# Kernel optimization log

Measured on AMD Instinct MI355X. Metric: run time of the kernel, lower is better.

Reference implementation:

```python
import jax, jax.numpy as jnp
import numpy as np

DIM = 512
HID = 4 * DIM
E = 8
B, T = 2, 2048


def setup_inputs() -> dict:
    key = jax.random.key(0)
    ks = jax.random.split(key, 8)
    s = 0.02
    x = jax.random.normal(ks[0], (B, T, DIM), dtype=jnp.float32)
    route = jax.random.randint(ks[1], (B * T,), 0, E, dtype=jnp.int32)
    # stacked per-expert params; Linear y = x @ W + b with W in [in, out] layout
    w_in = jax.random.normal(ks[2], (E, DIM, HID), dtype=jnp.float32) * s
    b_in = jnp.zeros((E, HID), dtype=jnp.float32)
    w_gate = jax.random.normal(ks[3], (E, DIM, HID), dtype=jnp.float32) * s
    b_gate = jnp.zeros((E, HID), dtype=jnp.float32)
    w_out = jax.random.normal(ks[4], (E, HID, DIM), dtype=jnp.float32) * s
    b_out = jnp.zeros((E, DIM), dtype=jnp.float32)
    return {"x": x, "route": route, "w_in": w_in, "b_in": b_in,
            "w_gate": w_gate, "b_gate": b_gate, "w_out": w_out, "b_out": b_out}


def reference(x, route, w_in, b_in, w_gate, b_gate, w_out, b_out):
    Bb, Tt, C = x.shape
    xf = x.reshape(-1, C)  # [N, C]
    out = jnp.zeros_like(xf)
    n_experts = w_in.shape[0]
    # loop over the small fixed expert set; each expert is a SwiGLU FFN,
    # output scattered back by masking (same math as output[idx] += expert(x[idx]))
    for e in range(n_experts):
        mask = (route == e).astype(xf.dtype)[:, None]  # [N, 1]
        h = jax.nn.silu(xf @ w_gate[e] + b_gate[e]) * (xf @ w_in[e] + b_in[e])  # [N, 4C]
        out = out + mask * (h @ w_out[e] + b_out[e])
    return out.reshape(Bb, Tt, C)
```

## Files before the change

### kernel.cpp

```cpp
#include <hip/hip_runtime.h>

#define DIM 512
#define HID 2048
#define NEXP 8

typedef __attribute__((ext_vector_type(8))) short v8s;
typedef __attribute__((ext_vector_type(4))) float v4f;

__device__ __forceinline__ unsigned short f2bf(float f) {
  union { __bf16 b; unsigned short u; } c;
  c.b = (__bf16)f;
  return c.u;
}

__device__ __forceinline__ void gload16(const void* g, void* l) {
  __builtin_amdgcn_global_load_lds(
      (const __attribute__((address_space(1))) unsigned int*)g,
      (__attribute__((address_space(3))) unsigned int*)l, 16, 0, 0);
}

__global__ void route_prep(const int* __restrict__ route, int* __restrict__ meta, int ntok) {
  __shared__ int c[NEXP];
  int t = threadIdx.x;
  if (t < NEXP) c[t] = 0;
  __syncthreads();
  for (int n = t; n < ntok; n += blockDim.x) atomicAdd(&c[route[n]], 1);
  __syncthreads();
  if (t == 0) {
    int acc = 0, pacc = 0;
    for (int e = 0; e < NEXP; ++e) {
      meta[e] = c[e];
      meta[NEXP + e] = acc;
      meta[2 * NEXP + e] = acc;
      meta[3 * NEXP + e] = pacc;
      acc += c[e];
      pacc += ((c[e] + 127) >> 7) << 7;
    }
  }
}

__global__ void fill_perm(const int* __restrict__ route, int* __restrict__ meta,
                          int* __restrict__ perm, int ntok) {
  int n = blockIdx.x * blockDim.x + threadIdx.x;
  if (n < ntok) {
    int p = atomicAdd(&meta[2 * NEXP + route[n]], 1);
    perm[p] = n;
  }
}


__global__ __launch_bounds__(256) void wgi_conv(
    const float* __restrict__ wg, const float* __restrict__ wi,
    unsigned short* __restrict__ wgp, unsigned short* __restrict__ wip)
{
  const int s = blockIdx.x;
  const int j = blockIdx.y;
  const int e = blockIdx.z >> 1;
  const int which = blockIdx.z & 1;
  const float* src = (which ? wi : wg) + (size_t)e * DIM * HID;
  unsigned short* dst = (which ? wip : wgp) + (((size_t)e * 16 + j) * 8 + s) * 8192;
  const int t = threadIdx.x;
  #pragma unroll
  for (int i = 0; i < 4; ++i) {
    const int c = t + 256 * i;
    const int kq = c >> 7, n = c & 127;
    const float* srow = src + (size_t)(s * 64 + kq * 8) * HID + j * 128 + n;
    v8s r;
    #pragma unroll
    for (int q = 0; q < 8; ++q) r[q] = (short)f2bf(srow[(size_t)q * HID]);
    *(v8s*)(dst + (size_t)c * 8) = r;
  }
}

__global__ __launch_bounds__(256) void wo_conv(
    const float* __restrict__ wo, unsigned short* __restrict__ wop)
{
  const int s = blockIdx.x;
  const int j = blockIdx.y;
  const int e = blockIdx.z;
  const float* src = wo + (size_t)e * HID * DIM;
  unsigned short* dst = wop + (((size_t)e * 8 + j) * 32 + s) * 4096;
  const int t = threadIdx.x;
  #pragma unroll
  for (int i = 0; i < 2; ++i) {
    const int c = t + 256 * i;
    const int kq = c >> 6, n = c & 63;
    const float* srow = src + (size_t)(s * 64 + kq * 8) * DIM + j * 64 + n;
    v8s r;
    #pragma unroll
    for (int q = 0; q < 8; ++q) r[q] = (short)f2bf(srow[(size_t)q * DIM]);
    *(v8s*)(dst + (size_t)c * 8) = r;
  }
}

__global__ __launch_bounds__(256, 2) void gemm1(
    const float* __restrict__ x,
    const unsigned short* __restrict__ wgp, const float* __restrict__ bg_,
    const unsigned short* __restrict__ wip, const float* __restrict__ bi_,
    const int* __restrict__ meta, const int* __restrict__ perm,
    unsigned short* __restrict__ hbuf)
{
  const int bid = blockIdx.x;
  const int e = bid & 7;
  const int r_ = bid >> 3;
  const int j = r_ & 15;
  const int mt = r_ >> 4;
  const int cnt = meta[e];
  const int m0 = mt * 128;
  if (m0 >= cnt) return;
  const int off  = meta[NEXP + e];
  const int poff = meta[3 * NEXP + e];
  const int n0 = j * 128;

  __shared__ __align__(16) unsigned char lds[49152];

  const int t = threadIdx.x;
  const int l = t & 63, w = t >> 6;
  const int wm = w >> 1, wn = w & 1;
  const int fr = l & 15, fg = l >> 4;

  const int ar = t >> 1, ah = t & 1;
  int arow = m0 + ar; if (arow >= cnt) arow = cnt - 1;
  const float* asrc = x + (size_t)perm[off + arow] * DIM + ah * 16;

  const unsigned short* pg = wgp + ((size_t)e * 16 + j) * 65536;
  const unsigned short* pi = wip + ((size_t)e * 16 + j) * 65536;

  v4f accG[4][4], accI[4][4];
  #pragma unroll
  for (int i = 0; i < 4; ++i)
    #pragma unroll
    for (int q = 0; q < 4; ++q) {
      accG[i][q] = (v4f){0.f, 0.f, 0.f, 0.f};
      accI[i][q] = (v4f){0.f, 0.f, 0.f, 0.f};
    }

  auto stage_w = [&](int s, int b) {
    unsigned char* base = lds + b * 24576;
    const unsigned short* pgs = pg + (size_t)s * 4096;
    const unsigned short* pis = pi + (size_t)s * 4096;
    gload16(pgs + t * 8,        base + 8192 + w * 1024);
    gload16(pgs + 2048 + t * 8, base + 8192 + 4096 + w * 1024);
    gload16(pis + t * 8,        base + 16384 + w * 1024);
    gload16(pis + 2048 + t * 8, base + 16384 + 4096 + w * 1024);
  };

  float4 a0, a1, a2, a3;
  auto stage_a_load = [&](int s) {
    const float4* p = (const float4*)(asrc + s * 32);
    a0 = p[0]; a1 = p[1]; a2 = p[2]; a3 = p[3];
  };
  auto stage_a_write = [&](int b) {
    unsigned char* base = lds + b * 24576;
    v8s r0, r1;
    r0[0] = (short)f2bf(a0.x); r0[1] = (short)f2bf(a0.y);
    r0[2] = (short)f2bf(a0.z); r0[3] = (short)f2bf(a0.w);
    r0[4] = (short)f2bf(a1.x); r0[5] = (short)f2bf(a1.y);
    r0[6] = (short)f2bf(a1.z); r0[7] = (short)f2bf(a1.w);
    r1[0] = (short)f2bf(a2.x); r1[1] = (short)f2bf(a2.y);
    r1[2] = (short)f2bf(a2.z); r1[3] = (short)f2bf(a2.w);
    r1[4] = (short)f2bf(a3.x); r1[5] = (short)f2bf(a3.y);
    r1[6] = (short)f2bf(a3.z); r1[7] = (short)f2bf(a3.w);
    *(v8s*)(base + ((ah * 2 + 0) * 128 + ar) * 16) = r0;
    *(v8s*)(base + ((ah * 2 + 1) * 128 + ar) * 16) = r1;
  };

  stage_w(0, 0);
  stage_a_load(0);
  stage_a_write(0);
  __syncthreads();

  int cur = 0;
  for (int s = 0; s < 16; ++s) {
    if (s < 15) {
      stage_w(s + 1, cur ^ 1);
      stage_a_load(s + 1);
    }
    unsigned char* base = lds + cur * 24576;
    v8s af[4], gf[4], inf[4];
    #pragma unroll
    for (int mf = 0; mf < 4; ++mf)
      af[mf] = *(const v8s*)(base + (fg * 128 + wm * 64 + mf * 16 + fr) * 16);
    #pragma unroll
    for (int nf = 0; nf < 4; ++nf) {
      gf[nf]  = *(const v8s*)(base + 8192  + (fg * 128 + wn * 64 + nf * 16 + fr) * 16);
      inf[nf] = *(const v8s*)(base + 16384 + (fg * 128 + wn * 64 + nf * 16 + fr) * 16);
    }
    #pragma unroll
    for (int mf = 0; mf < 4; ++mf)
      #pragma unroll
      for (int nf = 0; nf < 4; ++nf) {
        accG[mf][nf] = __builtin_amdgcn_mfma_f32_16x16x32_bf16(af[mf], gf[nf],  accG[mf][nf], 0, 0, 0);
        accI[mf][nf] = __builtin_amdgcn_mfma_f32_16x16x32_bf16(af[mf], inf[nf], accI[mf][nf], 0, 0, 0);
      }
    if (s < 15) stage_a_write(cur ^ 1);
    __syncthreads();
    cur ^= 1;
  }

  #pragma unroll
  for (int nf = 0; nf < 4; ++nf) {
    const int c = n0 + wn * 64 + nf * 16 + fr;
    const float bg = bg_[(size_t)e * HID + c];
    const float bi = bi_[(size_t)e * HID + c];
    #pragma unroll
    for (int mf = 0; mf < 4; ++mf)
      #pragma unroll
      for (int jj = 0; jj < 4; ++jj) {
        const int r = wm * 64 + mf * 16 + fg * 4 + jj;
        if (m0 + r < cnt) {
          const float g = accG[mf][nf][jj] + bg;
          const float v = accI[mf][nf][jj] + bi;
          const float hval = g / (1.f + __expf(-g)) * v;
          const int grow = poff + m0 + r;
          hbuf[(size_t)(grow >> 6) * 131072 + ((size_t)(c >> 3) * 64 + (grow & 63)) * 8 + (c & 7)] = f2bf(hval);
        }
      }
  }
}

__global__ __launch_bounds__(256, 4) void gemm2(
    const unsigned short* __restrict__ hbuf,
    const unsigned short* __restrict__ wop, const float* __restrict__ bo_,
    const int* __restrict__ meta, const int* __restrict__ perm,
    float* __restrict__ out)
{
  const int bid = blockIdx.x;
  const int e = bid & 7;
  const int r_ = bid >> 3;
  const int jn = r_ & 7;
  const int mt = r_ >> 3;
  const int cnt = meta[e];
  const int m0 = mt * 64;
  if (m0 >= cnt) return;
  const int off  = meta[NEXP + e];
  const int poff = meta[3 * NEXP + e];
  const int n0 = jn * 64;

  __shared__ __align__(16) unsigned char lds[32768];

  const int t = threadIdx.x;
  const int l = t & 63, w = t >> 6;
  const int wm = w >> 1, wn = w & 1;
  const int fr = l & 15, fg = l >> 4;

  const unsigned short* pa = hbuf + (size_t)((poff + m0) >> 6) * 131072;
  const unsigned short* pb = wop + ((size_t)e * 8 + jn) * 131072;

  v4f acc[2][2];
  #pragma unroll
  for (int i = 0; i < 2; ++i)
    #pragma unroll
    for (int q = 0; q < 2; ++q) acc[i][q] = (v4f){0.f, 0.f, 0.f, 0.f};

  auto stage = [&](int s, int b) {
    unsigned char* base = lds + b * 16384;
    const unsigned short* pas = pa + (size_t)s * 4096;
    const unsigned short* pbs = pb + (size_t)s * 4096;
    gload16(pas + t * 8,        base + w * 1024);
    gload16(pas + 2048 + t * 8, base + 4096 + w * 1024);
    gload16(pbs + t * 8,        base + 8192 + w * 1024);
    gload16(pbs + 2048 + t * 8, base + 8192 + 4096 + w * 1024);
  };

  stage(0, 0);
  __syncthreads();

  int cur = 0;
  for (int s = 0; s < 32; ++s) {
    if (s < 31) stage(s + 1, cur ^ 1);
    unsigned char* base = lds + cur * 16384;
    v8s af[2][2], bf2[2][2];
    #pragma unroll
    for (int kk = 0; kk < 2; ++kk) {
      #pragma unroll
      for (int mf = 0; mf < 2; ++mf)
        af[kk][mf]  = *(const v8s*)(base + ((kk * 4 + fg) * 64 + wm * 32 + mf * 16 + fr) * 16);
      #pragma unroll
      for (int nf = 0; nf < 2; ++nf)
        bf2[kk][nf] = *(const v8s*)(base + 8192 + ((kk * 4 + fg) * 64 + wn * 32 + nf * 16 + fr) * 16);
    }
    #pragma unroll
    for (int kk = 0; kk < 2; ++kk)
      #pragma unroll
      for (int mf = 0; mf < 2; ++mf)
        #pragma unroll
        for (int nf = 0; nf < 2; ++nf)
          acc[mf][nf] = __builtin_amdgcn_mfma_f32_16x16x32_bf16(af[kk][mf], bf2[kk][nf], acc[mf][nf], 0, 0, 0);
    __syncthreads();
    cur ^= 1;
  }

  #pragma unroll
  for (int nf = 0; nf < 2; ++nf) {
    const int c = n0 + wn * 32 + nf * 16 + fr;
    const float bo = bo_[(size_t)e * DIM + c];
    #pragma unroll
    for (int mf = 0; mf < 2; ++mf)
      #pragma unroll
      for (int jj = 0; jj < 4; ++jj) {
        const int r = wm * 32 + mf * 16 + fg * 4 + jj;
        if (m0 + r < cnt)
          out[(size_t)perm[off + m0 + r] * DIM + c] = acc[mf][nf][jj] + bo;
      }
  }
}

extern "C" void kernel_launch(void* const* d_in, const int* in_sizes, int n_in,
                              void* d_out, int out_size, void* d_ws, size_t ws_size,
                              hipStream_t stream) {
  const float* x      = (const float*)d_in[0];
  const int*   route  = (const int*)d_in[1];
  const float* w_in   = (const float*)d_in[2];
  const float* b_in   = (const float*)d_in[3];
  const float* w_gate = (const float*)d_in[4];
  const float* b_gate = (const float*)d_in[5];
  const float* w_out  = (const float*)d_in[6];
  const float* b_out  = (const float*)d_in[7];
  float* out = (float*)d_out;

  const int ntok = in_sizes[1];

  int* meta = (int*)d_ws;
  int* perm = (int*)((char*)d_ws + 128);

  const size_t WGP_OFF = 32768;
  const size_t WMAT_BYTES = (size_t)NEXP * DIM * HID * 2;

  unsigned short* wgp  = (unsigned short*)((char*)d_ws + WGP_OFF);
  unsigned short* wip  = (unsigned short*)((char*)d_ws + WGP_OFF + WMAT_BYTES);
  unsigned short* wop  = (unsigned short*)((char*)d_ws + WGP_OFF + 2 * WMAT_BYTES);
  unsigned short* hbuf = (unsigned short*)((char*)d_ws + WGP_OFF + 3 * WMAT_BYTES);

  const int MT1 = (ntok + 127) / 128;
  const int MT2 = (ntok + 63) / 64;

  route_prep<<<1, 256, 0, stream>>>(route, meta, ntok);
  fill_perm<<<(ntok + 255) / 256, 256, 0, stream>>>(route, meta, perm, ntok);
  wgi_conv<<<dim3(8, 16, 16), 256, 0, stream>>>(w_gate, w_in, wgp, wip);
  wo_conv<<<dim3(32, 8, 8), 256, 0, stream>>>(w_out, wop);
  gemm1<<<NEXP * 16 * MT1, 256, 0, stream>>>(
      x, wgp, b_gate, wip, b_in, meta, perm, hbuf);
  gemm2<<<NEXP * 8 * MT2, 256, 0, stream>>>(
      hbuf, wop, b_out, meta, perm, out);
}
```

Before: 126.2 us.

## Pre-gather tokens to bf16, shrink gemm1 M tile, widen gemm2 to 8 waves

Adds an x_conv kernel that gathers the routed tokens and converts them to packed bf16 once, so gemm1 can stream A through async global-to-LDS loads instead of per-block fp32 loads and conversions. gemm1 drops from 128-row to 64-row tiles with a smaller LDS footprint and higher occupancy bound, giving more blocks. gemm2 now runs 512 threads with one n-fragment per wave. The xp buffer reuses the wop workspace, so wo_conv is reordered to run after gemm1, which serialises that conversion behind the first GEMM.

Measured after the change: 112.9 us. -10.5%, faster.

```diff
diff --git a/kernel.cpp b/kernel.cpp
--- a/kernel.cpp
+++ b/kernel.cpp
@@ -93,11 +93,40 @@
   }
 }
 
-__global__ __launch_bounds__(256, 2) void gemm1(
-    const float* __restrict__ x,
+__global__ __launch_bounds__(256) void x_conv(
+    const float* __restrict__ x, const int* __restrict__ meta,
+    const int* __restrict__ perm, unsigned short* __restrict__ xp)
+{
+  const int bid = blockIdx.x;
+  const int e = bid & 7;
+  const int mt = bid >> 3;
+  const int cnt = meta[e];
+  if (mt * 64 >= cnt) return;
+  const int off  = meta[NEXP + e];
+  const int poff = meta[3 * NEXP + e];
+  const int t = threadIdx.x;
+  const int r = t & 63, q = t >> 6;
+  int arow = mt * 64 + r; if (arow >= cnt) arow = cnt - 1;
+  const float* src = x + (size_t)perm[off + arow] * DIM + q * 128;
+  unsigned short* dst = xp + (size_t)((poff + mt * 64) >> 6) * 32768;
+  #pragma unroll
+  for (int j = 0; j < 16; ++j) {
+    float4 f0 = ((const float4*)src)[2 * j];
+    float4 f1 = ((const float4*)src)[2 * j + 1];
+    v8s v;
+    v[0] = (short)f2bf(f0.x); v[1] = (short)f2bf(f0.y);
+    v[2] = (short)f2bf(f0.z); v[3] = (short)f2bf(f0.w);
+    v[4] = (short)f2bf(f1.x); v[5] = (short)f2bf(f1.y);
+    v[6] = (short)f2bf(f1.z); v[7] = (short)f2bf(f1.w);
+    *(v8s*)(dst + (size_t)((q * 16 + j) * 64 + r) * 8) = v;
+  }
+}
+
+__global__ __launch_bounds__(256, 4) void gemm1(
+    const unsigned short* __restrict__ xp,
     const unsigned short* __restrict__ wgp, const float* __restrict__ bg_,
     const unsigned short* __restrict__ wip, const float* __restrict__ bi_,
-    const int* __restrict__ meta, const int* __restrict__ perm,
+    const int* __restrict__ meta,
     unsigned short* __restrict__ hbuf)
 {
   const int bid = blockIdx.x;
@@ -106,120 +135,89 @@
   const int j = r_ & 15;
   const int mt = r_ >> 4;
   const int cnt = meta[e];
-  const int m0 = mt * 128;
+  const int m0 = mt * 64;
   if (m0 >= cnt) return;
-  const int off  = meta[NEXP + e];
   const int poff = meta[3 * NEXP + e];
   const int n0 = j * 128;
 
-  __shared__ __align__(16) unsigned char lds[49152];
+  __shared__ __align__(16) unsigned char lds[40960];
 
   const int t = threadIdx.x;
   const int l = t & 63, w = t >> 6;
   const int wm = w >> 1, wn = w & 1;
   const int fr = l & 15, fg = l >> 4;
 
-  const int ar = t >> 1, ah = t & 1;
-  int arow = m0 + ar; if (arow >= cnt) arow = cnt - 1;
-  const float* asrc = x + (size_t)perm[off + arow] * DIM + ah * 16;
-
+  const unsigned short* pa = xp + (size_t)((poff + m0) >> 6) * 32768;
   const unsigned short* pg = wgp + ((size_t)e * 16 + j) * 65536;
   const unsigned short* pi = wip + ((size_t)e * 16 + j) * 65536;
 
-  v4f accG[4][4], accI[4][4];
-  #pragma unroll
-  for (int i = 0; i < 4; ++i)
+  v4f accG[2][4], accI[2][4];
+  #pragma unroll
+  for (int i = 0; i < 2; ++i)
     #pragma unroll
     for (int q = 0; q < 4; ++q) {
       accG[i][q] = (v4f){0.f, 0.f, 0.f, 0.f};
       accI[i][q] = (v4f){0.f, 0.f, 0.f, 0.f};
     }
 
-  auto stage_w = [&](int s, int b) {
-    unsigned char* base = lds + b * 24576;
-    const unsigned short* pgs = pg + (size_t)s * 4096;
-    const unsigned short* pis = pi + (size_t)s * 4096;
-    gload16(pgs + t * 8,        base + 8192 + w * 1024);
-    gload16(pgs + 2048 + t * 8, base + 8192 + 4096 + w * 1024);
-    gload16(pis + t * 8,        base + 16384 + w * 1024);
-    gload16(pis + 2048 + t * 8, base + 16384 + 4096 + w * 1024);
+  auto stage = [&](int s, int b) {
+    unsigned char* base = lds + b * 20480;
+    gload16(pa + (size_t)s * 2048 + t * 8,        base + w * 1024);
+    gload16(pg + (size_t)s * 4096 + t * 8,        base + 4096 + w * 1024);
+    gload16(pg + (size_t)s * 4096 + 2048 + t * 8, base + 8192 + w * 1024);
+    gload16(pi + (size_t)s * 4096 + t * 8,        base + 12288 + w * 1024);
+    gload16(pi + (size_t)s * 4096 + 2048 + t * 8, base + 16384 + w * 1024);
   };
 
-  float4 a0, a1, a2, a3;
-  auto stage_a_load = [&](int s) {
-    const float4* p = (const float4*)(asrc + s * 32);
-    a0 = p[0]; a1 = p[1]; a2 = p[2]; a3 = p[3];
-  };
-  auto stage_a_write = [&](int b) {
-    unsigned char* base = lds + b * 24576;
-    v8s r0, r1;
-    r0[0] = (short)f2bf(a0.x); r0[1] = (short)f2bf(a0.y);
-    r0[2] = (short)f2bf(a0.z); r0[3] = (short)f2bf(a0.w);
-    r0[4] = (short)f2bf(a1.x); r0[5] = (short)f2bf(a1.y);
-    r0[6] = (short)f2bf(a1.z); r0[7] = (short)f2bf(a1.w);
-    r1[0] = (short)f2bf(a2.x); r1[1] = (short)f2bf(a2.y);
-    r1[2] = (short)f2bf(a2.z); r1[3] = (short)f2bf(a2.w);
-    r1[4] = (short)f2bf(a3.x); r1[5] = (short)f2bf(a3.y);
-    r1[6] = (short)f2bf(a3.z); r1[7] = (short)f2bf(a3.w);
-    *(v8s*)(base + ((ah * 2 + 0) * 128 + ar) * 16) = r0;
-    *(v8s*)(base + ((ah * 2 + 1) * 128 + ar) * 16) = r1;
-  };
-
-  stage_w(0, 0);
-  stage_a_load(0);
-  stage_a_write(0);
+  stage(0, 0);
   __syncthreads();
 
   int cur = 0;
   for (int s = 0; s < 16; ++s) {
-    if (s < 15) {
-      stage_w(s + 1, cur ^ 1);
-      stage_a_load(s + 1);
-    }
-    unsigned char* base = lds + cur * 24576;
-    v8s af[4], gf[4], inf[4];
-    #pragma unroll
-    for (int mf = 0; mf < 4; ++mf)
-      af[mf] = *(const v8s*)(base + (fg * 128 + wm * 64 + mf * 16 + fr) * 16);
+    if (s < 15) stage(s + 1, cur ^ 1);
+    unsigned char* base = lds + cur * 20480;
+    v8s af[2], gf[4], inf[4];
+    #pragma unroll
+    for (int mf = 0; mf < 2; ++mf)
+      af[mf] = *(const v8s*)(base + ((fg * 64) + wm * 32 + mf * 16 + fr) * 16);
     #pragma unroll
     for (int nf = 0; nf < 4; ++nf) {
-      gf[nf]  = *(const v8s*)(base + 8192  + (fg * 128 + wn * 64 + nf * 16 + fr) * 16);
-      inf[nf] = *(const v8s*)(base + 16384 + (fg * 128 + wn * 64 + nf * 16 + fr) * 16);
-    }
-    #pragma unroll
-    for (int mf = 0; mf < 4; ++mf)
+      gf[nf]  = *(const v8s*)(base + 4096  + ((fg * 128) + wn * 64 + nf * 16 + fr) * 16);
+      inf[nf] = *(const v8s*)(base + 12288 + ((fg * 128) + wn * 64 + nf * 16 + fr) * 16);
+    }
+    #pragma unroll
+    for (int mf = 0; mf < 2; ++mf)
       #pragma unroll
       for (int nf = 0; nf < 4; ++nf) {
         accG[mf][nf] = __builtin_amdgcn_mfma_f32_16x16x32_bf16(af[mf], gf[nf],  accG[mf][nf], 0, 0, 0);
         accI[mf][nf] = __builtin_amdgcn_mfma_f32_16x16x32_bf16(af[mf], inf[nf], accI[mf][nf], 0, 0, 0);
       }
-    if (s < 15) stage_a_write(cur ^ 1);
     __syncthreads();
     cur ^= 1;
   }
 
+  const size_t tbase = (size_t)((poff + m0) >> 6) * 131072;
   #pragma unroll
   for (int nf = 0; nf < 4; ++nf) {
     const int c = n0 + wn * 64 + nf * 16 + fr;
     const float bg = bg_[(size_t)e * HID + c];
     const float bi = bi_[(size_t)e * HID + c];
     #pragma unroll
-    for (int mf = 0; mf < 4; ++mf)
+    for (int mf = 0; mf < 2; ++mf)
       #pragma unroll
       for (int jj = 0; jj < 4; ++jj) {
-        const int r = wm * 64 + mf * 16 + fg * 4 + jj;
+        const int r = wm * 32 + mf * 16 + fg * 4 + jj;
         if (m0 + r < cnt) {
           const float g = accG[mf][nf][jj] + bg;
           const float v = accI[mf][nf][jj] + bi;
           const float hval = g / (1.f + __expf(-g)) * v;
-          const int grow = poff + m0 + r;
-          hbuf[(size_t)(grow >> 6) * 131072 + ((size_t)(c >> 3) * 64 + (grow & 63)) * 8 + (c & 7)] = f2bf(hval);
+          hbuf[tbase + (size_t)((c >> 3) * 64 + r) * 8 + (c & 7)] = f2bf(hval);
         }
       }
   }
 }
 
-__global__ __launch_bounds__(256, 4) void gemm2(
+__global__ __launch_bounds__(512, 4) void gemm2(
     const unsigned short* __restrict__ hbuf,
     const unsigned short* __restrict__ wop, const float* __restrict__ bo_,
     const int* __restrict__ meta, const int* __restrict__ perm,
@@ -241,26 +239,20 @@
 
   const int t = threadIdx.x;
   const int l = t & 63, w = t >> 6;
-  const int wm = w >> 1, wn = w & 1;
+  const int wm = w >> 2, wn = w & 3;
   const int fr = l & 15, fg = l >> 4;
 
   const unsigned short* pa = hbuf + (size_t)((poff + m0) >> 6) * 131072;
   const unsigned short* pb = wop + ((size_t)e * 8 + jn) * 131072;
 
-  v4f acc[2][2];
-  #pragma unroll
-  for (int i = 0; i < 2; ++i)
-    #pragma unroll
-    for (int q = 0; q < 2; ++q) acc[i][q] = (v4f){0.f, 0.f, 0.f, 0.f};
+  v4f acc[2];
+  acc[0] = (v4f){0.f, 0.f, 0.f, 0.f};
+  acc[1] = (v4f){0.f, 0.f, 0.f, 0.f};
 
   auto stage = [&](int s, int b) {
     unsigned char* base = lds + b * 16384;
-    const unsigned short* pas = pa + (size_t)s * 4096;
-    const unsigned short* pbs = pb + (size_t)s * 4096;
-    gload16(pas + t * 8,        base + w * 1024);
-    gload16(pas + 2048 + t * 8, base + 4096 + w * 1024);
-    gload16(pbs + t * 8,        base + 8192 + w * 1024);
-    gload16(pbs + 2048 + t * 8, base + 8192 + 4096 + w * 1024);
+    gload16(pa + (size_t)s * 4096 + t * 8, base + w * 1024);
+    gload16(pb + (size_t)s * 4096 + t * 8, base + 8192 + w * 1024);
   };
 
   stage(0, 0);
@@ -270,40 +262,33 @@
   for (int s = 0; s < 32; ++s) {
     if (s < 31) stage(s + 1, cur ^ 1);
     unsigned char* base = lds + cur * 16384;
-    v8s af[2][2], bf2[2][2];
+    v8s af[2][2], bf2[2];
     #pragma unroll
     for (int kk = 0; kk < 2; ++kk) {
       #pragma unroll
       for (int mf = 0; mf < 2; ++mf)
-        af[kk][mf]  = *(const v8s*)(base + ((kk * 4 + fg) * 64 + wm * 32 + mf * 16 + fr) * 16);
-      #pragma unroll
-      for (int nf = 0; nf < 2; ++nf)
-        bf2[kk][nf] = *(const v8s*)(base + 8192 + ((kk * 4 + fg) * 64 + wn * 32 + nf * 16 + fr) * 16);
+        af[kk][mf] = *(const v8s*)(base + ((kk * 4 + fg) * 64 + wm * 32 + mf * 16 + fr) * 16);
+      bf2[kk] = *(const v8s*)(base + 8192 + ((kk * 4 + fg) * 64 + wn * 16 + fr) * 16);
     }
     #pragma unroll
     for (int kk = 0; kk < 2; ++kk)
       #pragma unroll
       for (int mf = 0; mf < 2; ++mf)
-        #pragma unroll
-        for (int nf = 0; nf < 2; ++nf)
-          acc[mf][nf] = __builtin_amdgcn_mfma_f32_16x16x32_bf16(af[kk][mf], bf2[kk][nf], acc[mf][nf], 0, 0, 0);
+        acc[mf] = __builtin_amdgcn_mfma_f32_16x16x32_bf16(af[kk][mf], bf2[kk], acc[mf], 0, 0, 0);
     __syncthreads();
     cur ^= 1;
   }
 
-  #pragma unroll
-  for (int nf = 0; nf < 2; ++nf) {
-    const int c = n0 + wn * 32 + nf * 16 + fr;
-    const float bo = bo_[(size_t)e * DIM + c];
-    #pragma unroll
-    for (int mf = 0; mf < 2; ++mf)
-      #pragma unroll
-      for (int jj = 0; jj < 4; ++jj) {
-        const int r = wm * 32 + mf * 16 + fg * 4 + jj;
-        if (m0 + r < cnt)
-          out[(size_t)perm[off + m0 + r] * DIM + c] = acc[mf][nf][jj] + bo;
-      }
-  }
+  const int c = n0 + wn * 16 + fr;
+  const float bo = bo_[(size_t)e * DIM + c];
+  #pragma unroll
+  for (int mf = 0; mf < 2; ++mf)
+    #pragma unroll
+    for (int jj = 0; jj < 4; ++jj) {
+      const int r = wm * 32 + mf * 16 + fg * 4 + jj;
+      if (m0 + r < cnt)
+        out[(size_t)perm[off + m0 + r] * DIM + c] = acc[mf][jj] + bo;
+    }
 }
 
 extern "C" void kernel_launch(void* const* d_in, const int* in_sizes, int n_in,
@@ -330,17 +315,18 @@
   unsigned short* wgp  = (unsigned short*)((char*)d_ws + WGP_OFF);
   unsigned short* wip  = (unsigned short*)((char*)d_ws + WGP_OFF + WMAT_BYTES);
   unsigned short* wop  = (unsigned short*)((char*)d_ws + WGP_OFF + 2 * WMAT_BYTES);
+  unsigned short* xp   = wop;
   unsigned short* hbuf = (unsigned short*)((char*)d_ws + WGP_OFF + 3 * WMAT_BYTES);
 
-  const int MT1 = (ntok + 127) / 128;
-  const int MT2 = (ntok + 63) / 64;
+  const int MT64 = (ntok + 63) / 64;
 
   route_prep<<<1, 256, 0, stream>>>(route, meta, ntok);
   fill_perm<<<(ntok + 255) / 256, 256, 0, stream>>>(route, meta, perm, ntok);
+  x_conv<<<NEXP * MT64, 256, 0, stream>>>(x, meta, perm, xp);
   wgi_conv<<<dim3(8, 16, 16), 256, 0, stream>>>(w_gate, w_in, wgp, wip);
+  gemm1<<<NEXP * 16 * MT64, 256, 0, stream>>>(
+      xp, wgp, b_gate, wip, b_in, meta, hbuf);
   wo_conv<<<dim3(32, 8, 8), 256, 0, stream>>>(w_out, wop);
-  gemm1<<<NEXP * 16 * MT1, 256, 0, stream>>>(
-      x, wgp, b_gate, wip, b_in, meta, perm, hbuf);
-  gemm2<<<NEXP * 8 * MT2, 256, 0, stream>>>(
+  gemm2<<<NEXP * 8 * MT64, 512, 0, stream>>>(
       hbuf, wop, b_out, meta, perm, out);
 }
```
